# Kernel tuning notes

Measured on AMD Instinct MI355X. Metric: run time of the kernel, lower is better.

Reference implementation:

```python
import jax, jax.numpy as jnp
import numpy as np
from jax import lax

B, CIN, COUT, K = 256, 3, 16, 3
D, H, W_ = 16, 32, 32
POOL = 4


def setup_inputs() -> dict:
    key = jax.random.key(0)
    kx, kw, kb = jax.random.split(key, 3)
    x = jax.random.normal(kx, (B, CIN, D, H, W_), dtype=jnp.float32)
    # Conv3d default init scale ~ 1/sqrt(fan_in)
    fan_in = CIN * K * K * K
    bound = 1.0 / np.sqrt(fan_in)
    W = jax.random.uniform(kw, (COUT, CIN, K, K, K), dtype=jnp.float32, minval=-bound, maxval=bound)
    b = jax.random.uniform(kb, (COUT,), dtype=jnp.float32, minval=-bound, maxval=bound)
    return {"x": x, "W": W, "b": b}


def reference(x, W, b):
    # Conv3d, valid padding, stride 1: [B,16,14,30,30]
    y = lax.conv_general_dilated(
        x, W, window_strides=(1, 1, 1), padding="VALID",
        dimension_numbers=("NCDHW", "OIDHW", "NCDHW"))
    y = y + b[None, :, None, None, None]
    # channel softmax (dim=1)
    s = jax.nn.softmax(y, axis=1)
    # 4x4x4 max-pool, stride 4, no padding: [B,16,3,7,7]
    out = lax.reduce_window(
        s, -jnp.inf, lax.max,
        window_dimensions=(1, 1, POOL, POOL, POOL),
        window_strides=(1, 1, POOL, POOL, POOL),
        padding="VALID")
    return out
```

## Files before the change

kernel.cpp:

```cpp
#include <hip/hip_runtime.h>
#include <math.h>

#define BATCH 256
#define CIN   3
#define COUT  16
#define DI    16
#define HI    32
#define WI    32

typedef _Float16 f16;
typedef f16   f16x4 __attribute__((ext_vector_type(4)));
typedef f16   f16x8 __attribute__((ext_vector_type(8)));
typedef float f32x4 __attribute__((ext_vector_type(4)));

#define ROWU   144
#define PLANEU 4320
#define XS_N   (6 * PLANEU)
#define G8OFF  (2 * PLANEU + 2 * ROWU)

#define SV8(a, b) __builtin_shufflevector(a, b, 0, 1, 2, 3, 4, 5, 6, 7)

__global__ __launch_bounds__(256, 3) void conv_sm_pool_mfma(
    const float* __restrict__ x, const float* __restrict__ W,
    const float* __restrict__ bias, float* __restrict__ out)
{
    __shared__ __align__(16) f16 xs[XS_N];

    const int tid  = threadIdx.x;
    const int lane = tid & 63;
    const int wave = tid >> 6;
    const int b    = blockIdx.x / 3;
    const int pd   = blockIdx.x % 3;
    const int d0   = pd * 4;

    const int col = lane & 15;
    const int q   = lane >> 4;

    const float* wc = W + col * 81;
    const float* wq = wc + q * 6;
    f16x8 wm[3];
    #pragma unroll
    for (int kw = 0; kw < 3; ++kw) {
        #pragma unroll
        for (int j = 0; j < 8; ++j) {
            const int ci = j & 3, jj = j >> 2;
            float v = (ci < 3) ? wq[ci * 27 + 3 * jj + kw] : 0.f;
            wm[kw][j] = (f16)v;
        }
    }
    f16x8 wg = {};
    if (q == 0) {
        #pragma unroll
        for (int j = 0; j < 8; ++j) {
            const int ci = j & 3, kw = j >> 2;
            if (ci < 3) wg[j] = (f16)wc[ci * 27 + 24 + kw];
        }
    } else if (q == 1) {
        #pragma unroll
        for (int j = 0; j < 3; ++j) wg[j] = (f16)wc[j * 27 + 26];
    }
    const float4 bv = *(const float4*)(bias + q * 4);

    for (int i = tid; i < 1440; i += 256) {
        int wqd = i & 7;
        int r   = i >> 3;
        int hh  = r % 30;
        int dd  = r / 30;
        const float* px = x + ((size_t)b * 48 + (d0 + dd)) * 1024 + hh * 32 + wqd * 4;
        float4 a0 = *(const float4*)(px);
        float4 a1 = *(const float4*)(px + 16384);
        float4 a2 = *(const float4*)(px + 32768);
        f16x8 p0, p1;
        p0[0] = (f16)a0.x; p0[1] = (f16)a1.x; p0[2] = (f16)a2.x; p0[3] = (f16)0.f;
        p0[4] = (f16)a0.y; p0[5] = (f16)a1.y; p0[6] = (f16)a2.y; p0[7] = (f16)0.f;
        p1[0] = (f16)a0.z; p1[1] = (f16)a1.z; p1[2] = (f16)a2.z; p1[3] = (f16)0.f;
        p1[4] = (f16)a0.w; p1[5] = (f16)a1.w; p1[6] = (f16)a2.w; p1[7] = (f16)0.f;
        f16* dst = xs + ((dd * 30 + hh) * 36 + wqd * 4) * 4;
        *(f16x8*)(dst)     = p0;
        *(f16x8*)(dst + 8) = p1;
    }

    const int g0   = q * 2;
    const int off1 = (g0 / 3) * PLANEU + (g0 % 3) * ROWU;
    const int off2 = ((g0 + 1) / 3) * PLANEU + ((g0 + 1) % 3) * ROWU;
    const int hl = col >> 2, wl = col & 3;
    const int spat  = hl * ROWU + wl * 4;
    const int g8sel = (q == 0) ? 0 : 8;

    __syncthreads();

    for (int cell = wave; cell < 49; cell += 4) {
        const int ch = cell / 7;
        const int pw = cell - ch * 7;
        const f16* base = xs + (ch * 4) * ROWU + pw * 16 + spat;

        f16x4 A1[4][3], A2[4][3], GA[4], GB[4];
        #pragma unroll
        for (int d = 0; d < 4; ++d) {
            const f16* rb = base + d * PLANEU;
            #pragma unroll
            for (int kw = 0; kw < 3; ++kw) {
                A1[d][kw] = *(const f16x4*)(rb + off1 + kw * 4);
                A2[d][kw] = *(const f16x4*)(rb + off2 + kw * 4);
            }
            GA[d] = *(const f16x4*)(rb + G8OFF + g8sel);
            GB[d] = *(const f16x4*)(rb + G8OFF + g8sel + 4);
        }

        f32x4 acc[4];
        #pragma unroll
        for (int d = 0; d < 4; ++d) {
            f32x4 a = {0.f, 0.f, 0.f, 0.f};
            a = __builtin_amdgcn_mfma_f32_16x16x32_f16(wm[0], SV8(A1[d][0], A2[d][0]), a, 0, 0, 0);
            a = __builtin_amdgcn_mfma_f32_16x16x32_f16(wm[1], SV8(A1[d][1], A2[d][1]), a, 0, 0, 0);
            a = __builtin_amdgcn_mfma_f32_16x16x32_f16(wm[2], SV8(A1[d][2], A2[d][2]), a, 0, 0, 0);
            a = __builtin_amdgcn_mfma_f32_16x16x32_f16(wg,   SV8(GA[d],    GB[d]),    a, 0, 0, 0);
            acc[d] = a;
        }

        f32x4 pm = {0.f, 0.f, 0.f, 0.f};
        #pragma unroll
        for (int d = 0; d < 4; ++d) {
            float y0 = acc[d][0] + bv.x, y1 = acc[d][1] + bv.y;
            float y2 = acc[d][2] + bv.z, y3 = acc[d][3] + bv.w;
            float e0 = __expf(y0), e1 = __expf(y1), e2 = __expf(y2), e3 = __expf(y3);
            float s = (e0 + e1) + (e2 + e3);
            s += __shfl_xor(s, 16);
            s += __shfl_xor(s, 32);
            float inv = __builtin_amdgcn_rcpf(s);
            pm[0] = fmaxf(pm[0], e0 * inv);
            pm[1] = fmaxf(pm[1], e1 * inv);
            pm[2] = fmaxf(pm[2], e2 * inv);
            pm[3] = fmaxf(pm[3], e3 * inv);
        }

        #pragma unroll
        for (int m = 1; m <= 8; m <<= 1) {
            pm[0] = fmaxf(pm[0], __shfl_xor(pm[0], m));
            pm[1] = fmaxf(pm[1], __shfl_xor(pm[1], m));
            pm[2] = fmaxf(pm[2], __shfl_xor(pm[2], m));
            pm[3] = fmaxf(pm[3], __shfl_xor(pm[3], m));
        }

        if (col == 0) {
            float* po = out + ((size_t)b * COUT + q * 4) * 147 + pd * 49 + cell;
            po[0]   = pm[0];
            po[147] = pm[1];
            po[294] = pm[2];
            po[441] = pm[3];
        }
    }
}

extern "C" void kernel_launch(void* const* d_in, const int* in_sizes, int n_in,
                              void* d_out, int out_size, void* d_ws, size_t ws_size,
                              hipStream_t stream) {
    const float* x    = (const float*)d_in[0];
    const float* W    = (const float*)d_in[1];
    const float* bias = (const float*)d_in[2];
    float* out = (float*)d_out;

    conv_sm_pool_mfma<<<BATCH * 3, 256, 0, stream>>>(x, W, bias, out);
}
```

Baseline: 35.32 us.

## Split input staging in two halves and overlap second load with first-plane MFMAs

```diff
diff --git a/kernel.cpp b/kernel.cpp
--- a/kernel.cpp
+++ b/kernel.cpp
@@ -19,6 +19,36 @@
 #define G8OFF  (2 * PLANEU + 2 * ROWU)
 
 #define SV8(a, b) __builtin_shufflevector(a, b, 0, 1, 2, 3, 4, 5, 6, 7)
+#define MFMA16(A, B, C) __builtin_amdgcn_mfma_f32_16x16x32_f16(A, B, C, 0, 0, 0)
+
+#define ITER(pmv, D, HL, SPAT)  do {                                          \
+    const f16* rb_ = xs + (D) * PLANEU + (HL) * ROWU + (SPAT);                \
+    f16x4 b10_ = *(const f16x4*)(rb_ + off1);                                 \
+    f16x4 b20_ = *(const f16x4*)(rb_ + off2);                                 \
+    f16x4 b11_ = *(const f16x4*)(rb_ + off1 + 4);                             \
+    f16x4 b21_ = *(const f16x4*)(rb_ + off2 + 4);                             \
+    f16x4 b12_ = *(const f16x4*)(rb_ + off1 + 8);                             \
+    f16x4 b22_ = *(const f16x4*)(rb_ + off2 + 8);                             \
+    f16x4 ga_  = *(const f16x4*)(rb_ + G8OFF + g8sel);                        \
+    f16x4 gb_  = *(const f16x4*)(rb_ + G8OFF + g8sel + 4);                    \
+    f32x4 a_ = {0.f, 0.f, 0.f, 0.f};                                          \
+    a_ = MFMA16(wm[0], SV8(b10_, b20_), a_);                                  \
+    a_ = MFMA16(wm[1], SV8(b11_, b21_), a_);                                  \
+    a_ = MFMA16(wm[2], SV8(b12_, b22_), a_);                                  \
+    a_ = MFMA16(wg,    SV8(ga_,  gb_),  a_);                                  \
+    float y0_ = a_[0] + bv.x, y1_ = a_[1] + bv.y;                             \
+    float y2_ = a_[2] + bv.z, y3_ = a_[3] + bv.w;                             \
+    float e0_ = __expf(y0_), e1_ = __expf(y1_);                               \
+    float e2_ = __expf(y2_), e3_ = __expf(y3_);                               \
+    float s_ = (e0_ + e1_) + (e2_ + e3_);                                     \
+    s_ += __shfl_xor(s_, 16);                                                 \
+    s_ += __shfl_xor(s_, 32);                                                 \
+    float inv_ = __builtin_amdgcn_rcpf(s_);                                   \
+    pmv[0] = fmaxf(pmv[0], e0_ * inv_);                                       \
+    pmv[1] = fmaxf(pmv[1], e1_ * inv_);                                       \
+    pmv[2] = fmaxf(pmv[2], e2_ * inv_);                                       \
+    pmv[3] = fmaxf(pmv[3], e3_ * inv_);                                       \
+} while (0)
 
 __global__ __launch_bounds__(256, 3) void conv_sm_pool_mfma(
     const float* __restrict__ x, const float* __restrict__ W,
@@ -36,15 +66,15 @@
     const int col = lane & 15;
     const int q   = lane >> 4;
 
-    const float* wc = W + col * 81;
-    const float* wq = wc + q * 6;
+    const float* wc  = W + col * 81;
+    const float* wqp = wc + q * 6;
     f16x8 wm[3];
     #pragma unroll
     for (int kw = 0; kw < 3; ++kw) {
         #pragma unroll
         for (int j = 0; j < 8; ++j) {
             const int ci = j & 3, jj = j >> 2;
-            float v = (ci < 3) ? wq[ci * 27 + 3 * jj + kw] : 0.f;
+            float v = (ci < 3) ? wqp[ci * 27 + 3 * jj + kw] : 0.f;
             wm[kw][j] = (f16)v;
         }
     }
@@ -61,7 +91,7 @@
     }
     const float4 bv = *(const float4*)(bias + q * 4);
 
-    for (int i = tid; i < 1440; i += 256) {
+    for (int i = tid; i < 720; i += 256) {
         int wqd = i & 7;
         int r   = i >> 3;
         int hh  = r % 30;
@@ -79,75 +109,99 @@
         *(f16x8*)(dst)     = p0;
         *(f16x8*)(dst + 8) = p1;
     }
+    if (tid < 180) {
+        f16x8 z = {};
+        f16* pz = xs + tid * ROWU + 128;
+        *(f16x8*)(pz)     = z;
+        *(f16x8*)(pz + 8) = z;
+    }
 
     const int g0   = q * 2;
     const int off1 = (g0 / 3) * PLANEU + (g0 % 3) * ROWU;
     const int off2 = ((g0 + 1) / 3) * PLANEU + ((g0 + 1) % 3) * ROWU;
-    const int hl = col >> 2, wl = col & 3;
-    const int spat  = hl * ROWU + wl * 4;
+    const int cc = (col >> 3) & 1;
+    const int ww = (col >> 2) & 1;
+    const int wl = col & 3;
     const int g8sel = (q == 0) ? 0 : 8;
+    const int pw  = 2 * wave + ww;
+    const int wb4 = (pw * 4 + wl) * 4;
+    int spati[4];
+    #pragma unroll
+    for (int i = 0; i < 4; ++i) {
+        int ch = 2 * i + cc;
+        if (ch > 6) ch = 6;
+        spati[i] = ch * 4 * ROWU + wb4;
+    }
 
     __syncthreads();
 
-    for (int cell = wave; cell < 49; cell += 4) {
-        const int ch = cell / 7;
-        const int pw = cell - ch * 7;
-        const f16* base = xs + (ch * 4) * ROWU + pw * 16 + spat;
-
-        f16x4 A1[4][3], A2[4][3], GA[4], GB[4];
-        #pragma unroll
-        for (int d = 0; d < 4; ++d) {
-            const f16* rb = base + d * PLANEU;
+    float4 ra0[3], ra1[3], ra2[3];
+    #pragma unroll
+    for (int j = 0; j < 3; ++j) {
+        int t = tid + 256 * j;
+        if (t < 720) {
+            int wqd = t & 7, r = t >> 3;
+            int hh = r % 30, dd = 3 + r / 30;
+            const float* px = x + ((size_t)b * 48 + (d0 + dd)) * 1024 + hh * 32 + wqd * 4;
+            ra0[j] = *(const float4*)(px);
+            ra1[j] = *(const float4*)(px + 16384);
+            ra2[j] = *(const float4*)(px + 32768);
+        }
+    }
+
+    f32x4 pm[4];
+    #pragma unroll
+    for (int i = 0; i < 4; ++i) pm[i] = (f32x4){0.f, 0.f, 0.f, 0.f};
+
+    #pragma unroll
+    for (int i = 0; i < 4; ++i) {
+        #pragma unroll
+        for (int hl = 0; hl < 4; ++hl) ITER(pm[i], 0, hl, spati[i]);
+    }
+
+    #pragma unroll
+    for (int j = 0; j < 3; ++j) {
+        int t = tid + 256 * j;
+        if (t < 720) {
+            int wqd = t & 7, r = t >> 3;
+            int hh = r % 30, dd = 3 + r / 30;
+            f16x8 p0, p1;
+            p0[0] = (f16)ra0[j].x; p0[1] = (f16)ra1[j].x; p0[2] = (f16)ra2[j].x; p0[3] = (f16)0.f;
+            p0[4] = (f16)ra0[j].y; p0[5] = (f16)ra1[j].y; p0[6] = (f16)ra2[j].y; p0[7] = (f16)0.f;
+            p1[0] = (f16)ra0[j].z; p1[1] = (f16)ra1[j].z; p1[2] = (f16)ra2[j].z; p1[3] = (f16)0.f;
+            p1[4] = (f16)ra0[j].w; p1[5] = (f16)ra1[j].w; p1[6] = (f16)ra2[j].w; p1[7] = (f16)0.f;
+            f16* dst = xs + ((dd * 30 + hh) * 36 + wqd * 4) * 4;
+            *(f16x8*)(dst)     = p0;
+            *(f16x8*)(dst + 8) = p1;
+        }
+    }
+    __syncthreads();
+
+    #pragma unroll
+    for (int i = 0; i < 4; ++i) {
+        #pragma unroll
+        for (int d = 1; d < 4; ++d) {
             #pragma unroll
-            for (int kw = 0; kw < 3; ++kw) {
-                A1[d][kw] = *(const f16x4*)(rb + off1 + kw * 4);
-                A2[d][kw] = *(const f16x4*)(rb + off2 + kw * 4);
-            }
-            GA[d] = *(const f16x4*)(rb + G8OFF + g8sel);
-            GB[d] = *(const f16x4*)(rb + G8OFF + g8sel + 4);
-        }
-
-        f32x4 acc[4];
-        #pragma unroll
-        for (int d = 0; d < 4; ++d) {
-            f32x4 a = {0.f, 0.f, 0.f, 0.f};
-            a = __builtin_amdgcn_mfma_f32_16x16x32_f16(wm[0], SV8(A1[d][0], A2[d][0]), a, 0, 0, 0);
-            a = __builtin_amdgcn_mfma_f32_16x16x32_f16(wm[1], SV8(A1[d][1], A2[d][1]), a, 0, 0, 0);
-            a = __builtin_amdgcn_mfma_f32_16x16x32_f16(wm[2], SV8(A1[d][2], A2[d][2]), a, 0, 0, 0);
-            a = __builtin_amdgcn_mfma_f32_16x16x32_f16(wg,   SV8(GA[d],    GB[d]),    a, 0, 0, 0);
-            acc[d] = a;
-        }
-
-        f32x4 pm = {0.f, 0.f, 0.f, 0.f};
-        #pragma unroll
-        for (int d = 0; d < 4; ++d) {
-            float y0 = acc[d][0] + bv.x, y1 = acc[d][1] + bv.y;
-            float y2 = acc[d][2] + bv.z, y3 = acc[d][3] + bv.w;
-            float e0 = __expf(y0), e1 = __expf(y1), e2 = __expf(y2), e3 = __expf(y3);
-            float s = (e0 + e1) + (e2 + e3);
-            s += __shfl_xor(s, 16);
-            s += __shfl_xor(s, 32);
-            float inv = __builtin_amdgcn_rcpf(s);
-            pm[0] = fmaxf(pm[0], e0 * inv);
-            pm[1] = fmaxf(pm[1], e1 * inv);
-            pm[2] = fmaxf(pm[2], e2 * inv);
-            pm[3] = fmaxf(pm[3], e3 * inv);
-        }
-
-        #pragma unroll
-        for (int m = 1; m <= 8; m <<= 1) {
-            pm[0] = fmaxf(pm[0], __shfl_xor(pm[0], m));
-            pm[1] = fmaxf(pm[1], __shfl_xor(pm[1], m));
-            pm[2] = fmaxf(pm[2], __shfl_xor(pm[2], m));
-            pm[3] = fmaxf(pm[3], __shfl_xor(pm[3], m));
-        }
-
-        if (col == 0) {
-            float* po = out + ((size_t)b * COUT + q * 4) * 147 + pd * 49 + cell;
-            po[0]   = pm[0];
-            po[147] = pm[1];
-            po[294] = pm[2];
-            po[441] = pm[3];
+            for (int hl = 0; hl < 4; ++hl) ITER(pm[i], d, hl, spati[i]);
+        }
+    }
+
+    #pragma unroll
+    for (int i = 0; i < 4; ++i) {
+        #pragma unroll
+        for (int r = 0; r < 4; ++r) {
+            float v = pm[i][r];
+            v = fmaxf(v, __shfl_xor(v, 1));
+            v = fmaxf(v, __shfl_xor(v, 2));
+            pm[i][r] = v;
+        }
+        const int ch = 2 * i + cc;
+        if (wl == 0 && ch < 7 && pw < 7) {
+            float* po = out + ((size_t)b * COUT + q * 4) * 147 + pd * 49 + ch * 7 + pw;
+            po[0]   = pm[i][0];
+            po[147] = pm[i][1];
+            po[294] = pm[i][2];
+            po[441] = pm[i][3];
         }
     }
 }
```

New measurement: 64.10 us. +81.5%, slower.
